# Kernel tuning notes

Measured on AMD Instinct MI355X. Metric: run time of the kernel, lower is better.

## Reference

```python
import jax, jax.numpy as jnp
import numpy as np

SIGMA = 1.0   # noise std (unit-variance synthetic input)
P = 11        # patch size p1
K = 16        # number of similar patches k1
WIN = 65      # search window w (odd)
S = 3         # reference-patch stride
ALPHA = 0.5   # n2n alpha


def _unfold(x, ksize, stride):
    # (N,1,H,W) -> (N, ksize*ksize, Ho, Wo); kernel positions row-major (== torch F.unfold for C=1)
    return jax.lax.conv_general_dilated_patches(
        x, (ksize, ksize), (stride, stride), 'VALID',
        dimension_numbers=('NCHW', 'OIHW', 'NCHW'))


def block_matching(x, k, p, w, s):
    N, _, H, W = x.shape
    v = w // 2
    assert (H - p + 1) % s == 1 and (W - p + 1) % s == 1  # no edge-case branches needed
    Href = (H - p) // s + 1
    Wref = (W - p) // s + 1
    x_pad = jnp.pad(x, ((0, 0), (0, 0), (v, v), (v, v)))  # zero pad; invalid candidates masked below
    # |patch|^2 / p^2 at every position of the padded image (== F.avg_pool2d(x**2, p))
    sq = jax.lax.reduce_window(x_pad * x_pad, 0.0, jax.lax.add,
                               (1, 1, p, p), (1, 1, 1, 1), 'VALID') / (p * p)
    norms = _unfold(sq, 2 * v + 1, s)                                  # (N,(2v+1)^2,Href,Wref)
    norms = norms.reshape(N, 2 * v + 1, 2 * v + 1, Href, Wref).transpose(0, 3, 4, 1, 2)
    lw = _unfold(x_pad, 2 * v + p, s) / p                              # (N,(2v+p)^2,Href,Wref)
    lw = lw.reshape(N, 2 * v + p, 2 * v + p, Href, Wref).transpose(0, 3, 4, 1, 2)
    G = N * Href * Wref
    lw = lw.reshape(1, G, 2 * v + p, 2 * v + p)
    ref = lw[0, :, v:-v, v:-v][:, None]                                # (G,1,p,p) reference patches
    sp = jax.lax.conv_general_dilated(
        lw, ref, (1, 1), 'VALID',
        dimension_numbers=('NCHW', 'OIHW', 'NCHW'),
        feature_group_count=G)                                         # (1,G,2v+1,2v+1)
    dist = norms.reshape(1, G, 2 * v + 1, 2 * v + 1) - 2.0 * sp
    dist = dist.reshape(N, Href, Wref, 2 * v + 1, 2 * v + 1)
    # mask candidate patches that fall outside the original image (torch uses NaN padding + topk)
    offs = jnp.arange(-v, v + 1)
    hr = jnp.arange(Href) * s
    wr = jnp.arange(Wref) * s
    row_ok = (hr[:, None] + offs >= 0) & (hr[:, None] + offs <= H - p)  # (Href, 2v+1)
    col_ok = (wr[:, None] + offs >= 0) & (wr[:, None] + offs <= W - p)  # (Wref, 2v+1)
    valid = row_ok[:, None, :, None] & col_ok[None, :, None, :]
    dist = jnp.where(valid[None], dist, jnp.inf)
    dist = dist.at[..., v, v].set(-jnp.inf)                            # reference patch always kept
    dist = dist.reshape(N, Href, Wref, (2 * v + 1) ** 2)
    _, idx = jax.lax.top_k(-dist, k)                                   # k smallest distances
    ind_row = idx // (2 * v + 1) - v
    ind_col = idx % (2 * v + 1) - v
    ind = (ind_row + hr[None, :, None, None]) * (W - p + 1) + (ind_col + wr[None, None, :, None])
    return ind.reshape(N, -1)                                          # (N, Href*Wref*k)


def gather_groups(y, indices, k, p):
    N = y.shape[0]
    uf = _unfold(y, p, 1).reshape(N, p * p, -1)                        # (N, n, (H-p+1)(W-p+1))
    Yg = jnp.take_along_axis(uf, indices[:, None, :], axis=2)          # (N, n, L*k)
    L = indices.shape[1] // k
    return Yg.reshape(N, p * p, L, k).transpose(0, 2, 3, 1)            # (N, L, k, n)


def denoise1(Y, sigma):
    # method='n2n', constraints='affine'
    N, B, k, n = Y.shape
    D = n * sigma ** 2
    E = n * ALPHA ** 2 * sigma ** 2
    Ik = jnp.eye(k, dtype=Y.dtype)
    Q = Y @ jnp.swapaxes(Y, 2, 3) + E * Ik                             # (N,B,k,k), SPD
    Lc = jnp.linalg.cholesky(Q)
    Ikb = jnp.broadcast_to(Ik, Q.shape)
    Z = jax.scipy.linalg.solve_triangular(Lc, Ikb, lower=True)
    Qinv = jax.scipy.linalg.solve_triangular(jnp.swapaxes(Lc, 2, 3), Z, lower=False)
    Qinv1 = jnp.sum(Qinv, axis=3, keepdims=True)
    Qinv2 = jnp.sum(Qinv1, axis=2, keepdims=True)
    theta = Ik - (Qinv - (Qinv1 @ jnp.swapaxes(Qinv1, 2, 3)) / Qinv2) * (D + E)
    theta = jnp.swapaxes(theta, 2, 3)
    X_hat = theta @ Y
    weights = 1.0 / jnp.clip(jnp.sum(theta * theta, axis=3, keepdims=True), 1.0 / k, 1.0)
    return X_hat, weights


def _fold(x, H, W, p):
    # inverse of unfold: sum overlapping p x p patches back onto the image grid
    N, n, _ = x.shape
    Hp, Wp = H - p + 1, W - p + 1
    x = x.reshape(N, p, p, Hp, Wp)
    out = jnp.zeros((N, 1, H, W), x.dtype)
    for a in range(p):
        for b in range(p):
            out = out.at[:, 0, a:a + Hp, b:b + Wp].add(x[:, a, b])
    return out


def aggregate(X_hat, weights, indices, H, W, p):
    N, L, k, n = X_hat.shape
    X = (X_hat * weights).reshape(N, L * k, n).transpose(0, 2, 1)      # (N, n, L*k)
    Wt = jnp.broadcast_to(weights, (N, L, k, n)).reshape(N, L * k, n).transpose(0, 2, 1)
    Lfull = (H - p + 1) * (W - p + 1)
    def scat(vals, idx):
        return jnp.zeros((n, Lfull), vals.dtype).at[:, idx].add(vals)
    X_sum = jax.vmap(scat)(X, indices)
    W_sum = jax.vmap(scat)(Wt, indices)
    return _fold(X_sum, H, W, p) / _fold(W_sum, H, W, p)


def _forward(y):
    N, C, H, W = y.shape
    indices = block_matching(y, K, P, WIN, S)
    Yg = gather_groups(y, indices, K, P)
    X_hat, weights = denoise1(Yg, SIGMA)
    return aggregate(X_hat, weights, indices, H, W, P)


def setup_inputs():
    key = jax.random.key(0)
    y = jax.random.normal(key, (4, 1, 128, 128), dtype=jnp.float32)
    return {"y": y}


def reference(y):
    return _forward(y)
```

## Files before the change

kernel.cpp:

```cpp
#include <hip/hip_runtime.h>
#include <math.h>

#define HH 128
#define WW 128
#define NIMG 4
#define PP 11
#define KSIM 16
#define STRIDE_S 3
#define VRAD 32
#define WINW 65
#define NTASK (WINW*9)
#define HREF 40
#define WREF 40
#define NPOS 118
#define WROWS 75
#define WPITCH 84
#define NGROUP (NIMG*HREF*WREF)
#define EPS_E 30.25f
#define DE_C 151.25f
#define INFD 3.0e38f
#define RTASK (VRAD*9 + VRAD/8)

__global__ __launch_bounds__(256, 4)
void bm_kernel(const float* __restrict__ y, int* __restrict__ inds)
{
    __shared__ float win[WROWS][WPITCH];
    __shared__ float swv[4];
    __shared__ int   swi[4];

    const int blk = blockIdx.x;
    const int n   = blk / (HREF*WREF);
    const int rem = blk % (HREF*WREF);
    const int hr  = (rem / WREF) * STRIDE_S;
    const int wr  = (rem % WREF) * STRIDE_S;
    const float* img = y + n * HH * WW;
    const int tid = threadIdx.x;

    for (int t = tid; t < WROWS * WPITCH; t += 256) {
        int r = t / WPITCH, c = t % WPITCH;
        int gr = hr - VRAD + r, gc = wr - VRAD + c;
        float v = 0.f;
        if (c < WROWS && gr >= 0 && gr < HH && gc >= 0 && gc < WW)
            v = img[gr * WW + gc];
        win[r][c] = v;
    }
    __syncthreads();

    float d[3][8];
#pragma unroll
    for (int s = 0; s < 3; s++)
#pragma unroll
        for (int c = 0; c < 8; c++) d[s][c] = INFD;

#pragma unroll
    for (int s = 0; s < 3; s++) {
        int task = tid + (s << 8);
        if (task < NTASK) {
            int drx = task / 9;
            int c0  = (task % 9) * 8;
            int rr  = hr + drx - VRAD;
            bool rowok = (rr >= 0 && rr <= HH - PP);
            if (rowok) {
                float dot[8];
                float colsq[18];
#pragma unroll
                for (int c = 0; c < 8; c++) dot[c] = 0.f;
#pragma unroll
                for (int j2 = 0; j2 < 18; j2++) colsq[j2] = 0.f;
                for (int a = 0; a < PP; a++) {
                    const float* wrow = &win[drx + a][c0];
                    const float* rrow = &win[VRAD + a][VRAD];
                    float wv[18];
#pragma unroll
                    for (int j2 = 0; j2 < 18; j2++) wv[j2] = wrow[j2];
#pragma unroll
                    for (int j2 = 0; j2 < 18; j2++) colsq[j2] += wv[j2] * wv[j2];
#pragma unroll
                    for (int b = 0; b < PP; b++) {
                        float rv = rrow[b];
#pragma unroll
                        for (int c = 0; c < 8; c++)
                            dot[c] += wv[b + c] * rv;
                    }
                }
#pragma unroll
                for (int j2 = 1; j2 < 18; j2++) colsq[j2] += colsq[j2 - 1];
#pragma unroll
                for (int c = 0; c < 8; c++) {
                    int dcx = c0 + c;
                    int cc  = wr + dcx - VRAD;
                    float norm = colsq[c + 10] - (c ? colsq[c - 1] : 0.f);
                    if (dcx < WINW && cc >= 0 && cc <= WW - PP)
                        d[s][c] = norm - 2.f * dot[c];
                }
            }
            if (task == RTASK) d[s][0] = -INFD;
        }
    }

    float lval = INFD; int lidx = 0;
#pragma unroll
    for (int s = 0; s < 3; s++)
#pragma unroll
        for (int c = 0; c < 8; c++)
            if (d[s][c] < lval) { lval = d[s][c]; lidx = (s << 3) | c; }

    for (int sel = 0; sel < KSIM; sel++) {
        float rv = lval;
        int   ri = ((tid + ((lidx >> 3) << 8)) << 3) | (lidx & 7);
#pragma unroll
        for (int off = 32; off > 0; off >>= 1) {
            float ov = __shfl_down(rv, off);
            int   oi = __shfl_down(ri, off);
            if (ov < rv) { rv = ov; ri = oi; }
        }
        if ((tid & 63) == 0) { swv[tid >> 6] = rv; swi[tid >> 6] = ri; }
        __syncthreads();
        float bval = swv[0]; int bidx = swi[0];
#pragma unroll
        for (int w2 = 1; w2 < 4; w2++)
            if (swv[w2] < bval) { bval = swv[w2]; bidx = swi[w2]; }
        if (tid == 0) {
            int task = bidx >> 3;
            int drx = task / 9, dcx = (task % 9) * 8 + (bidx & 7);
            int prr = hr + drx - VRAD, pcc = wr + dcx - VRAD;
            inds[blk * KSIM + sel] = prr * NPOS + pcc;
        }
        __syncthreads();
        int otid = (bidx >> 3) & 255;
        if (tid == otid) {
            int code = (((bidx >> 3) >> 8) << 3) | (bidx & 7);
            lval = INFD; lidx = 0;
#pragma unroll
            for (int s = 0; s < 3; s++)
#pragma unroll
                for (int c = 0; c < 8; c++) {
                    if (((s << 3) | c) == code) d[s][c] = INFD;
                    if (d[s][c] < lval) { lval = d[s][c]; lidx = (s << 3) | c; }
                }
        }
    }
}

__global__ __launch_bounds__(256)
void dn_kernel(const float* __restrict__ y, const int* __restrict__ inds,
               float2* __restrict__ nd, int R)
{
    __shared__ float Ys[KSIM][122];
    __shared__ float Qs[KSIM][KSIM];
    __shared__ float Qinvs[KSIM][KSIM];
    __shared__ float thetas[KSIM][KSIM];
    __shared__ float s1[KSIM];
    __shared__ float ws16[KSIM];
    __shared__ float s2s;
    __shared__ int prow[KSIM], pcol[KSIM];

    const int g = (int)(((long long)blockIdx.x * 2753) % NGROUP);
    const int n = g / (HREF*WREF);
    const float* img = y + n * HH * WW;
    float2* ndI = nd + ((size_t)(blockIdx.x & (R - 1)) * NIMG + n) * HH * WW;
    const int tid = threadIdx.x;

    if (tid < KSIM) {
        int idx = inds[g * KSIM + tid];
        prow[tid] = idx / NPOS;
        pcol[tid] = idx % NPOS;
    }
    __syncthreads();

    for (int t = tid; t < KSIM * 121; t += 256) {
        int k = t / 121, jj = t % 121;
        int a = jj / PP, b = jj % PP;
        Ys[k][jj] = img[(prow[k] + a) * WW + pcol[k] + b];
    }
    __syncthreads();

    {
        int a = tid >> 4, b = tid & 15;
        float s = 0.f;
        for (int jj = 0; jj < 121; jj++)
            s += Ys[a][jj] * Ys[b][jj];
        if (a == b) s += EPS_E;
        Qs[a][b] = s;
    }
    __syncthreads();

    for (int c = 0; c < KSIM; c++) {
        if (tid == 0) Qs[c][c] = sqrtf(Qs[c][c]);
        __syncthreads();
        if (tid > c && tid < KSIM) Qs[tid][c] /= Qs[c][c];
        __syncthreads();
        {
            int a = tid >> 4, b = tid & 15;
            if (a > c && b > c && b <= a) Qs[a][b] -= Qs[a][c] * Qs[b][c];
        }
        __syncthreads();
    }

    if (tid < KSIM) {
        float z[KSIM];
#pragma unroll
        for (int r = 0; r < KSIM; r++) {
            float s = (r == tid) ? 1.f : 0.f;
#pragma unroll
            for (int m = 0; m < KSIM; m++)
                if (m < r) s -= Qs[r][m] * z[m];
            z[r] = s / Qs[r][r];
        }
#pragma unroll
        for (int r = KSIM - 1; r >= 0; r--) {
            float s = z[r];
#pragma unroll
            for (int m = 0; m < KSIM; m++)
                if (m > r) s -= Qs[m][r] * z[m];
            z[r] = s / Qs[r][r];
        }
#pragma unroll
        for (int r = 0; r < KSIM; r++) Qinvs[r][tid] = z[r];
    }
    __syncthreads();

    if (tid < KSIM) {
        float s = 0.f;
#pragma unroll
        for (int b = 0; b < KSIM; b++) s += Qinvs[tid][b];
        s1[tid] = s;
    }
    __syncthreads();
    if (tid == 0) {
        float s = 0.f;
#pragma unroll
        for (int a = 0; a < KSIM; a++) s += s1[a];
        s2s = s;
    }
    __syncthreads();

    {
        int a = tid >> 4, b = tid & 15;
        float th = ((a == b) ? 1.f : 0.f)
                 - (Qinvs[a][b] - s1[a] * s1[b] / s2s) * DE_C;
        thetas[a][b] = th;
    }
    __syncthreads();

    if (tid < KSIM) {
        float s = 0.f;
#pragma unroll
        for (int m = 0; m < KSIM; m++) s += thetas[m][tid] * thetas[m][tid];
        s = fminf(fmaxf(s, 1.f / (float)KSIM), 1.f);
        ws16[tid] = 1.f / s;
    }
    __syncthreads();

    for (int t = tid; t < KSIM * 121; t += 256) {
        int r = t / 121, jj = t % 121;
        float xh = 0.f;
#pragma unroll
        for (int m = 0; m < KSIM; m++) xh += thetas[m][r] * Ys[m][jj];
        float wv = ws16[r];
        int a = jj / PP, b = jj % PP;
        int px = (prow[r] + a) * WW + pcol[r] + b;
#if defined(__has_builtin) && __has_builtin(__builtin_amdgcn_global_atomic_fadd_v2f32)
        typedef float v2f __attribute__((ext_vector_type(2)));
        __builtin_amdgcn_global_atomic_fadd_v2f32((v2f*)&ndI[px], (v2f){wv * xh, wv});
#else
        atomicAdd(&ndI[px].x, wv * xh);
        atomicAdd(&ndI[px].y, wv);
#endif
    }
}

__global__ __launch_bounds__(256)
void fin_kernel(const float2* __restrict__ nd, float* __restrict__ out, int R)
{
    int t = blockIdx.x * 256 + threadIdx.x;
    if (t < NIMG * HH * WW) {
        float sn = 0.f, sd = 0.f;
        for (int r = 0; r < R; r++) {
            float2 v = nd[(size_t)r * NIMG * HH * WW + t];
            sn += v.x; sd += v.y;
        }
        out[t] = sn / sd;
    }
}

extern "C" void kernel_launch(void* const* d_in, const int* in_sizes, int n_in,
                              void* d_out, int out_size, void* d_ws, size_t ws_size,
                              hipStream_t stream)
{
    const float* y = (const float*)d_in[0];
    float* out = (float*)d_out;

    size_t indsBytes = (size_t)NGROUP * KSIM * sizeof(int);
    size_t perRep    = (size_t)NIMG * HH * WW * sizeof(float2);
    int R = 1;
    while (R < 4 && indsBytes + perRep * (size_t)(R * 2) <= ws_size) R <<= 1;

    float2* nd  = (float2*)d_ws;
    int*    inds = (int*)((char*)d_ws + perRep * (size_t)R);

    hipMemsetAsync(nd, 0, perRep * (size_t)R, stream);
    bm_kernel<<<NGROUP, 256, 0, stream>>>(y, inds);
    dn_kernel<<<NGROUP, 256, 0, stream>>>(y, inds, nd, R);
    fin_kernel<<<(NIMG * HH * WW + 255) / 256, 256, 0, stream>>>(nd, out, R);
}
```

Before: 524.2 us.

## Restructure denoise kernel: one group per 16 lanes, shuffle Cholesky, LDS tile accumulation

```diff
diff --git a/kernel.cpp b/kernel.cpp
--- a/kernel.cpp
+++ b/kernel.cpp
@@ -21,6 +21,11 @@
 #define INFD 3.0e38f
 #define RTASK (VRAD*9 + VRAD/8)
 
+#define TDIM 4
+#define NTIL (HREF/TDIM)
+#define FOOT 84
+#define FPITCH 85
+
 __global__ __launch_bounds__(256, 4)
 void bm_kernel(const float* __restrict__ y, int* __restrict__ inds)
 {
@@ -142,131 +147,148 @@
     }
 }
 
-__global__ __launch_bounds__(256)
+__global__ __launch_bounds__(256, 2)
 void dn_kernel(const float* __restrict__ y, const int* __restrict__ inds,
                float2* __restrict__ nd, int R)
 {
-    __shared__ float Ys[KSIM][122];
-    __shared__ float Qs[KSIM][KSIM];
-    __shared__ float Qinvs[KSIM][KSIM];
-    __shared__ float thetas[KSIM][KSIM];
-    __shared__ float s1[KSIM];
-    __shared__ float ws16[KSIM];
-    __shared__ float s2s;
-    __shared__ int prow[KSIM], pcol[KSIM];
-
-    const int g = (int)(((long long)blockIdx.x * 2753) % NGROUP);
-    const int n = g / (HREF*WREF);
+    __shared__ float2 acc[FOOT][FPITCH];
+
+    const int blk = blockIdx.x;
+    const int n  = blk / (NTIL*NTIL);
+    const int tr = blk % (NTIL*NTIL);
+    const int ti = tr / NTIL, tj = tr % NTIL;
+    const int tid = threadIdx.x;
+    const int r0 = 3*(ti*TDIM) - VRAD;
+    const int c0 = 3*(tj*TDIM) - VRAD;
     const float* img = y + n * HH * WW;
-    float2* ndI = nd + ((size_t)(blockIdx.x & (R - 1)) * NIMG + n) * HH * WW;
-    const int tid = threadIdx.x;
-
-    if (tid < KSIM) {
-        int idx = inds[g * KSIM + tid];
-        prow[tid] = idx / NPOS;
-        pcol[tid] = idx % NPOS;
+
+    {
+        float* af = (float*)acc;
+        for (int t = tid; t < FOOT*FPITCH*2; t += 256) af[t] = 0.f;
     }
     __syncthreads();
 
-    for (int t = tid; t < KSIM * 121; t += 256) {
-        int k = t / 121, jj = t % 121;
-        int a = jj / PP, b = jj % PP;
-        Ys[k][jj] = img[(prow[k] + a) * WW + pcol[k] + b];
+    const int wv2  = tid >> 6;
+    const int lane = tid & 63;
+    const int sg   = lane >> 4;
+    const int r    = lane & 15;
+    const int g    = n * (HREF*WREF) + (ti*TDIM + wv2) * WREF + (tj*TDIM + sg);
+
+    const int idx  = inds[g * KSIM + r];
+    const int prow = idx / NPOS, pcol = idx % NPOS;
+    const float* pbase = img + prow * WW + pcol;
+
+    float q[16];
+#pragma unroll
+    for (int m = 0; m < 16; m++) q[m] = (m == r) ? EPS_E : 0.f;
+    for (int a = 0; a < PP; a++) {
+        float yr[PP];
+#pragma unroll
+        for (int b = 0; b < PP; b++) yr[b] = pbase[a * WW + b];
+#pragma unroll
+        for (int b = 0; b < PP; b++) {
+            float yj = yr[b];
+#pragma unroll
+            for (int m = 0; m < 16; m++) {
+                float ym = __shfl(yj, m, 16);
+                q[m] += yj * ym;
+            }
+        }
+    }
+
+#pragma unroll
+    for (int c = 0; c < 16; c++) {
+        float dc = __shfl(q[c], c, 16);
+        float s  = sqrtf(dc);
+        float inv = 1.f / s;
+        q[c] = (r == c) ? s : q[c] * inv;
+#pragma unroll
+        for (int b = c + 1; b < 16; b++) {
+            float lb = __shfl(q[c], b, 16);
+            q[b] -= q[c] * lb;
+        }
+    }
+
+    float z[16];
+#pragma unroll
+    for (int rr = 0; rr < 16; rr++) {
+        float s = (rr == r) ? 1.f : 0.f;
+        float diag = 0.f;
+#pragma unroll
+        for (int m = 0; m <= rr; m++) {
+            float lrm = __shfl(q[m], rr, 16);
+            if (m < rr) s -= lrm * z[m];
+            else diag = lrm;
+        }
+        z[rr] = s / diag;
+    }
+    float x[16];
+#pragma unroll
+    for (int rr = 15; rr >= 0; rr--) {
+        float s = z[rr];
+        float diag = 0.f;
+#pragma unroll
+        for (int m = 15; m >= rr; m--) {
+            float lmr = __shfl(q[rr], m, 16);
+            if (m > rr) s -= lmr * x[m];
+            else diag = lmr;
+        }
+        x[rr] = s / diag;
+    }
+
+    float s1 = 0.f;
+#pragma unroll
+    for (int b = 0; b < 16; b++) s1 += x[b];
+    float s2 = s1;
+#pragma unroll
+    for (int mask = 1; mask < 16; mask <<= 1) s2 += __shfl_xor(s2, mask, 16);
+    float th[16], tsq = 0.f;
+#pragma unroll
+    for (int b = 0; b < 16; b++) {
+        float s1b = __shfl(s1, b, 16);
+        float t = ((b == r) ? 1.f : 0.f) - (x[b] - s1 * s1b / s2) * DE_C;
+        th[b] = t;
+        tsq += t * t;
+    }
+    tsq = fminf(fmaxf(tsq, 1.f / (float)KSIM), 1.f);
+    const float w = 1.f / tsq;
+
+    const int arow = prow - r0, acol = pcol - c0;
+    for (int a = 0; a < PP; a++) {
+        float yr[PP];
+#pragma unroll
+        for (int b = 0; b < PP; b++) yr[b] = pbase[a * WW + b];
+#pragma unroll
+        for (int b = 0; b < PP; b++) {
+            float yj = yr[b];
+            float xh = 0.f;
+#pragma unroll
+            for (int m = 0; m < 16; m++) {
+                float ym = __shfl(yj, m, 16);
+                xh += th[m] * ym;
+            }
+            float2* cell = &acc[arow + a][acol + b];
+            atomicAdd(&cell->x, w * xh);
+            atomicAdd(&cell->y, w);
+        }
     }
     __syncthreads();
 
-    {
-        int a = tid >> 4, b = tid & 15;
-        float s = 0.f;
-        for (int jj = 0; jj < 121; jj++)
-            s += Ys[a][jj] * Ys[b][jj];
-        if (a == b) s += EPS_E;
-        Qs[a][b] = s;
-    }
-    __syncthreads();
-
-    for (int c = 0; c < KSIM; c++) {
-        if (tid == 0) Qs[c][c] = sqrtf(Qs[c][c]);
-        __syncthreads();
-        if (tid > c && tid < KSIM) Qs[tid][c] /= Qs[c][c];
-        __syncthreads();
-        {
-            int a = tid >> 4, b = tid & 15;
-            if (a > c && b > c && b <= a) Qs[a][b] -= Qs[a][c] * Qs[b][c];
-        }
-        __syncthreads();
-    }
-
-    if (tid < KSIM) {
-        float z[KSIM];
-#pragma unroll
-        for (int r = 0; r < KSIM; r++) {
-            float s = (r == tid) ? 1.f : 0.f;
-#pragma unroll
-            for (int m = 0; m < KSIM; m++)
-                if (m < r) s -= Qs[r][m] * z[m];
-            z[r] = s / Qs[r][r];
-        }
-#pragma unroll
-        for (int r = KSIM - 1; r >= 0; r--) {
-            float s = z[r];
-#pragma unroll
-            for (int m = 0; m < KSIM; m++)
-                if (m > r) s -= Qs[m][r] * z[m];
-            z[r] = s / Qs[r][r];
-        }
-#pragma unroll
-        for (int r = 0; r < KSIM; r++) Qinvs[r][tid] = z[r];
-    }
-    __syncthreads();
-
-    if (tid < KSIM) {
-        float s = 0.f;
-#pragma unroll
-        for (int b = 0; b < KSIM; b++) s += Qinvs[tid][b];
-        s1[tid] = s;
-    }
-    __syncthreads();
-    if (tid == 0) {
-        float s = 0.f;
-#pragma unroll
-        for (int a = 0; a < KSIM; a++) s += s1[a];
-        s2s = s;
-    }
-    __syncthreads();
-
-    {
-        int a = tid >> 4, b = tid & 15;
-        float th = ((a == b) ? 1.f : 0.f)
-                 - (Qinvs[a][b] - s1[a] * s1[b] / s2s) * DE_C;
-        thetas[a][b] = th;
-    }
-    __syncthreads();
-
-    if (tid < KSIM) {
-        float s = 0.f;
-#pragma unroll
-        for (int m = 0; m < KSIM; m++) s += thetas[m][tid] * thetas[m][tid];
-        s = fminf(fmaxf(s, 1.f / (float)KSIM), 1.f);
-        ws16[tid] = 1.f / s;
-    }
-    __syncthreads();
-
-    for (int t = tid; t < KSIM * 121; t += 256) {
-        int r = t / 121, jj = t % 121;
-        float xh = 0.f;
-#pragma unroll
-        for (int m = 0; m < KSIM; m++) xh += thetas[m][r] * Ys[m][jj];
-        float wv = ws16[r];
-        int a = jj / PP, b = jj % PP;
-        int px = (prow[r] + a) * WW + pcol[r] + b;
+    float2* ndI = nd + ((size_t)(blk & (R - 1)) * NIMG + n) * HH * WW;
+    for (int t = tid; t < FOOT * FOOT; t += 256) {
+        int rr = t / FOOT, cc = t % FOOT;
+        float2 v = acc[rr][cc];
+        if (v.y != 0.f) {
+            int gr = r0 + rr, gc = c0 + cc;
+            int px = gr * WW + gc;
 #if defined(__has_builtin) && __has_builtin(__builtin_amdgcn_global_atomic_fadd_v2f32)
-        typedef float v2f __attribute__((ext_vector_type(2)));
-        __builtin_amdgcn_global_atomic_fadd_v2f32((v2f*)&ndI[px], (v2f){wv * xh, wv});
+            typedef float v2f __attribute__((ext_vector_type(2)));
+            __builtin_amdgcn_global_atomic_fadd_v2f32((v2f*)&ndI[px], (v2f){v.x, v.y});
 #else
-        atomicAdd(&ndI[px].x, wv * xh);
-        atomicAdd(&ndI[px].y, wv);
+            atomicAdd(&ndI[px].x, v.x);
+            atomicAdd(&ndI[px].y, v.y);
 #endif
+        }
     }
 }
 
@@ -301,6 +323,6 @@
 
     hipMemsetAsync(nd, 0, perRep * (size_t)R, stream);
     bm_kernel<<<NGROUP, 256, 0, stream>>>(y, inds);
-    dn_kernel<<<NGROUP, 256, 0, stream>>>(y, inds, nd, R);
+    dn_kernel<<<NIMG * NTIL * NTIL, 256, 0, stream>>>(y, inds, nd, R);
     fin_kernel<<<(NIMG * HH * WW + 255) / 256, 256, 0, stream>>>(nd, out, R);
 }
```

After: 476.6 us. 1.1x faster.
